# Kernel tuning notes

Measured on AMD Instinct MI355X. Metric: run time of the kernel, lower is better.

The kernel has to match this reference:

```python
import jax, jax.numpy as jnp
import numpy as np

DIM = 1024
N_SRC = 4096
N_TGT = 4096


def setup_inputs() -> dict:
    key = jax.random.key(0)
    ks = jax.random.split(key, 7)
    scale = 1.0 / np.sqrt(DIM)
    return {
        "source": jax.random.normal(ks[0], (N_SRC, DIM), dtype=jnp.float32),
        "target": jax.random.normal(ks[1], (N_TGT, DIM), dtype=jnp.float32),
        "W_src": jax.random.uniform(ks[2], (DIM, DIM), minval=-scale, maxval=scale, dtype=jnp.float32),
        "b_src": jax.random.uniform(ks[3], (DIM,), minval=-scale, maxval=scale, dtype=jnp.float32),
        "W_tgt": jax.random.uniform(ks[4], (DIM, DIM), minval=-scale, maxval=scale, dtype=jnp.float32),
        "b_tgt": jax.random.uniform(ks[5], (DIM,), minval=-scale, maxval=scale, dtype=jnp.float32),
        "temperature": jnp.array(1.0, dtype=jnp.float32),
    }


def reference(source, target, W_src, b_src, W_tgt, b_tgt, temperature):
    # Linear projections (torch Linear: x @ W.T + b)
    sp = source @ W_src.T + b_src            # [N, d]
    tp = target @ W_tgt.T + b_tgt            # [M, d]
    sq_s = jnp.sum(sp * sp, axis=-1, keepdims=True)   # [N, 1]
    sq_t = jnp.sum(tp * tp, axis=-1)                  # [M]
    d2 = sq_s + sq_t[None, :] - 2.0 * (sp @ tp.T)     # [N, M]
    cost = jnp.sqrt(jnp.maximum(d2, 0.0))
    # Softmin-style kernel, row-normalized over target entries
    K = jnp.exp(-cost / temperature)
    K = K / jnp.sum(K, axis=1, keepdims=True)
    aligned_source = K @ target                       # [N, d]
    return aligned_source, K
```

## Files before the change

kernel.cpp:

```cpp
#include <hip/hip_runtime.h>
#include <stdint.h>

#define DIM  1024
#define NSRC 4096
#define NTGT 4096

typedef __bf16 bf16_t;
typedef bf16_t bf16x8 __attribute__((ext_vector_type(8)));
typedef float  fx4    __attribute__((ext_vector_type(4)));

static __device__ __forceinline__ unsigned short f2bf(float f) {
  union { float f; uint32_t u; } v; v.f = f;
  return (unsigned short)((v.u + 0x7FFFu + ((v.u >> 16) & 1u)) >> 16);
}
static __device__ __forceinline__ float bf2f(unsigned short h) {
  union { uint32_t u; float f; } v; v.u = ((uint32_t)h) << 16;
  return v.f;
}

static __device__ __forceinline__ void gl_lds16(const unsigned short* g, unsigned short* l) {
  __builtin_amdgcn_global_load_lds(
      (__attribute__((address_space(1))) const void*)g,
      (__attribute__((address_space(3))) void*)l, 16, 0, 0);
}


__global__ void k_convert_all(const float* __restrict__ s, const float* __restrict__ t,
                              const float* __restrict__ w0, const float* __restrict__ w1,
                              unsigned short* __restrict__ sb, unsigned short* __restrict__ tb,
                              unsigned short* __restrict__ wb0, unsigned short* __restrict__ wb1) {
  int b = blockIdx.x;
  const float* in; unsigned short* out; int idx;
  if (b < 4096)      { in = s;  out = sb;  idx = b * 256 + threadIdx.x; }
  else if (b < 8192) { in = t;  out = tb;  idx = (b - 4096) * 256 + threadIdx.x; }
  else if (b < 9216) { in = w0; out = wb0; idx = (b - 8192) * 256 + threadIdx.x; }
  else               { in = w1; out = wb1; idx = (b - 9216) * 256 + threadIdx.x; }
  float4 v = ((const float4*)in)[idx];
  ushort4 o;
  o.x = f2bf(v.x); o.y = f2bf(v.y); o.z = f2bf(v.z); o.w = f2bf(v.w);
  ((ushort4*)out)[idx] = o;
}

__global__ void k_transpose_bf16(const float* __restrict__ in, unsigned short* __restrict__ out,
                                 int R, int C) {
  __shared__ unsigned short tile[32][33];
  int c0 = blockIdx.x * 32, r0 = blockIdx.y * 32;
  int tx = threadIdx.x, ty = threadIdx.y;
  for (int i = ty; i < 32; i += 8) {
    int row = r0 + i;
    int p = row & 63;
    int tr = (row & ~63) | ((p >> 2) | ((p & 3) << 4));
    tile[i][tx] = f2bf(in[(size_t)tr * C + c0 + tx]);
  }
  __syncthreads();
  for (int i = ty; i < 32; i += 8)
    out[(size_t)(c0 + i) * R + r0 + tx] = tile[tx][i];
}

__global__ void k_finalize(const float* __restrict__ P, float* __restrict__ aligned,
                           const unsigned short* __restrict__ Eb, float* __restrict__ Kf,
                           const float* __restrict__ rs) {
  const int b = blockIdx.x;
  const int lane = threadIdx.x & 63, w = threadIdx.x >> 6;
  const int src = ((lane & 15) << 2) | (lane >> 4);
  if (b < 4096) {
    const size_t stride = (size_t)NSRC * DIM;
#pragma unroll
    for (int it = 0; it < 4; ++it) {
      int idx = b * 16 + w * 4 + it;
      size_t base = (size_t)idx * 64;
      float r = 1.0f / rs[idx >> 4];
      float v = (P[base + lane] + P[base + stride + lane] +
                 P[base + 2 * stride + lane] + P[base + 3 * stride + lane]) * r;
      aligned[base + lane] = __shfl(v, src, 64);
    }
  } else {
    const int bb = b - 4096;
#pragma unroll
    for (int it = 0; it < 8; ++it) {
      int idx = bb * 32 + w * 8 + it;
      size_t base = (size_t)idx * 64;
      float r = 1.0f / rs[idx >> 6];
      float v = bf2f(Eb[base + lane]) * r;
      Kf[base + lane] = __shfl(v, src, 64);
    }
  }
}

template <int EPI>
__global__ void __launch_bounds__(256)
k_gemm(const unsigned short* __restrict__ A0, const unsigned short* __restrict__ B0,
       const unsigned short* __restrict__ A1, const unsigned short* __restrict__ B1,
       int N, int K,
       const float* __restrict__ bias0, const float* __restrict__ bias1,
       unsigned short* __restrict__ Cb0, unsigned short* __restrict__ Cb1,
       float* __restrict__ Cf,
       const float* __restrict__ sqs, const float* __restrict__ sqt,
       const float* __restrict__ tempPtr,
       float* __restrict__ red0, float* __restrict__ red1,
       int KS) {
  __shared__ unsigned short ldsA[128 * 32];
  __shared__ unsigned short ldsB[128 * 32];
  __shared__ float rsum[128];

  const unsigned short* A = A0;
  const unsigned short* B = B0;
  const float* bias = bias0;
  unsigned short* Cb = Cb0;
  float* red = red0;
  int k0 = 0, k1 = K;
  if constexpr (EPI == 0) {
    if (blockIdx.z) { A = A1; B = B1; bias = bias1; Cb = Cb1; red = red1; }
  }
  if constexpr (EPI == 3) { k0 = blockIdx.z * KS; k1 = k0 + KS; }

  const int m0 = blockIdx.y * 128;
  const int n0 = blockIdx.x * 128;
  const int tid  = threadIdx.x;
  const int lane = tid & 63;
  const int wv   = tid >> 6;
  const int wm   = wv >> 1, wn = wv & 1;

  const int c0    = wv * 2;
  const int srow  = lane >> 2;
  const int skoff = (lane & 3) * 8;
  const unsigned short* ag[2]; const unsigned short* bg[2];
  unsigned short* la[2]; unsigned short* lb[2];
#pragma unroll
  for (int j = 0; j < 2; ++j) {
    int c = c0 + j;
    ag[j] = A + (size_t)(m0 + c * 16 + srow) * K + skoff;
    bg[j] = B + (size_t)(n0 + c * 16 + srow) * K + skoff;
    la[j] = ldsA + c * 512;
    lb[j] = ldsB + c * 512;
  }

  const fx4 fzero = {0.f, 0.f, 0.f, 0.f};
  fx4 acc[4][4];
#pragma unroll
  for (int i = 0; i < 4; ++i)
#pragma unroll
    for (int j = 0; j < 4; ++j) acc[i][j] = fzero;

  const int frow = lane & 15;
  const int kq   = lane >> 4;
  const int aoff = (wm * 64 + frow) * 32 + kq * 8;
  const int boff = (wn * 64 + frow) * 32 + kq * 8;

  for (int ko = k0; ko < k1; ko += 32) {
    gl_lds16(ag[0] + ko, la[0]);
    gl_lds16(ag[1] + ko, la[1]);
    gl_lds16(bg[0] + ko, lb[0]);
    gl_lds16(bg[1] + ko, lb[1]);
    __syncthreads();
    bf16x8 af[4], bfr[4];
#pragma unroll
    for (int t = 0; t < 4; ++t) af[t]  = *(const bf16x8*)(ldsA + aoff + t * 512);
#pragma unroll
    for (int t = 0; t < 4; ++t) bfr[t] = *(const bf16x8*)(ldsB + boff + t * 512);
#pragma unroll
    for (int i = 0; i < 4; ++i)
#pragma unroll
      for (int j = 0; j < 4; ++j)
        acc[i][j] = __builtin_amdgcn_mfma_f32_16x16x32_bf16(af[i], bfr[j], acc[i][j], 0, 0, 0);
    __syncthreads();
  }

  const int gcol0 = n0 + wn * 64 + frow;
  const int scol  = n0 + wn * 64 + frow * 4;

  if constexpr (EPI == 0 || EPI == 1) {
    if (tid < 128) rsum[tid] = 0.f;
    __syncthreads();
    float invT = 0.f;
    if constexpr (EPI == 1) invT = 1.0f / tempPtr[0];
#pragma unroll
    for (int i = 0; i < 4; ++i)
#pragma unroll
      for (int r = 0; r < 4; ++r) {
        const int lrow = wm * 64 + kq * 4 + i * 16 + r;
        const int gm   = m0 + lrow;
        float si = 0.f;
        if constexpr (EPI == 1) si = sqs[gm];
        float racc = 0.f;
        ushort4 o;
        unsigned short* op = (unsigned short*)&o;
#pragma unroll
        for (int j = 0; j < 4; ++j) {
          float e;
          if constexpr (EPI == 0) {
            e = acc[i][j][r] + bias[gcol0 + j * 16];
          } else {
            float d2 = si + sqt[gcol0 + j * 16] - 2.0f * acc[i][j][r];
            float c = sqrtf(fmaxf(d2, 0.0f));
            e = __expf(-c * invT);
          }
          unsigned short eb = f2bf(e);
          op[j] = eb;
          float ev = bf2f(eb);
          racc += (EPI == 0) ? ev * ev : ev;
        }
        *(ushort4*)(Cb + (size_t)gm * N + scol) = o;
        racc += __shfl_xor(racc, 1, 64);
        racc += __shfl_xor(racc, 2, 64);
        racc += __shfl_xor(racc, 4, 64);
        racc += __shfl_xor(racc, 8, 64);
        if (frow == 0) atomicAdd(&rsum[lrow], racc);
      }
    __syncthreads();
    if (tid < 128) atomicAdd(&red[m0 + tid], rsum[tid]);
  } else {
    float* Pz = Cf + (size_t)blockIdx.z * NSRC * DIM;
#pragma unroll
    for (int i = 0; i < 4; ++i)
#pragma unroll
      for (int r = 0; r < 4; ++r) {
        const int gm = m0 + wm * 64 + kq * 4 + i * 16 + r;
        float4 v = make_float4(acc[i][0][r], acc[i][1][r], acc[i][2][r], acc[i][3][r]);
        *(float4*)(Pz + (size_t)gm * N + scol) = v;
      }
  }
}

extern "C" void kernel_launch(void* const* d_in, const int* in_sizes, int n_in,
                              void* d_out, int out_size, void* d_ws, size_t ws_size,
                              hipStream_t stream) {
  const float* source = (const float*)d_in[0];
  const float* target = (const float*)d_in[1];
  const float* W_src  = (const float*)d_in[2];
  const float* b_src  = (const float*)d_in[3];
  const float* W_tgt  = (const float*)d_in[4];
  const float* b_tgt  = (const float*)d_in[5];
  const float* temp   = (const float*)d_in[6];

  float* out     = (float*)d_out;
  float* aligned = out;
  float* Kout    = out + (size_t)NSRC * DIM;
  float* parts   = Kout;

  char* ws = (char*)d_ws;
  unsigned short* src_b  = (unsigned short*)(ws + 0);
  unsigned short* tgt_b  = (unsigned short*)(ws + 8388608);
  unsigned short* Wsrc_b = (unsigned short*)(ws + 16777216);
  unsigned short* Wtgt_b = (unsigned short*)(ws + 18874368);
  unsigned short* sp_b   = (unsigned short*)(ws + 20971520);
  unsigned short* tp_b   = (unsigned short*)(ws + 29360128);
  unsigned short* tgtT_b = (unsigned short*)(ws + 37748736);
  unsigned short* E_b    = (unsigned short*)(ws + 46137344);
  float* sq_s  = (float*)(ws + 79691776);
  float* sq_t  = (float*)(ws + 79708160);
  float* rsums = (float*)(ws + 79724544);

  hipMemsetAsync(sq_s, 0, 3 * NSRC * sizeof(float), stream);

  k_convert_all<<<10240, 256, 0, stream>>>(source, target, W_src, W_tgt,
                                           src_b, tgt_b, Wsrc_b, Wtgt_b);
  k_transpose_bf16<<<dim3(DIM / 32, NTGT / 32), dim3(32, 8), 0, stream>>>(target, tgtT_b, NTGT, DIM);

  k_gemm<0><<<dim3(DIM / 128, NSRC / 128, 2), 256, 0, stream>>>(
      src_b, Wsrc_b, tgt_b, Wtgt_b, DIM, DIM, b_src, b_tgt, sp_b, tp_b,
      nullptr, nullptr, nullptr, nullptr, sq_s, sq_t, 0);

  k_gemm<1><<<dim3(NTGT / 128, NSRC / 128, 1), 256, 0, stream>>>(
      sp_b, tp_b, nullptr, nullptr, NTGT, DIM, nullptr, nullptr, E_b, nullptr,
      nullptr, sq_s, sq_t, temp, rsums, nullptr, 0);

  k_gemm<3><<<dim3(DIM / 128, NSRC / 128, 4), 256, 0, stream>>>(
      E_b, tgtT_b, nullptr, nullptr, DIM, NTGT, nullptr, nullptr, nullptr, nullptr,
      parts, nullptr, nullptr, nullptr, nullptr, nullptr, NTGT / 4);

  k_finalize<<<12288, 256, 0, stream>>>(parts, aligned, E_b, Kout, rsums);
}
```

Measured before the change: 314.5 us.

## Add 256x256 pipelined score GEMM kernel and halve split-K for aligned GEMM

Replaces the generic 128x128 score GEMM (EPI==1) with a dedicated 512-thread, 256x256-tile kernel. It double-buffers LDS through direct global-to-LDS loads, interleaves staging with MFMA groups under explicit waitcnt and barrier control, and raises wave priority during MFMA. This aims at better data reuse and latency hiding for the largest GEMM. The K@target GEMM split-K drops from 4 to 2, which halves the partial-sum traffic, and the finalize step is split into two separate kernels. The tradeoffs are higher register and LDS pressure from the large tile, and fewer blocks for the split-K GEMM.

```diff
diff --git a/kernel.cpp b/kernel.cpp
--- a/kernel.cpp
+++ b/kernel.cpp
@@ -57,33 +57,34 @@
     out[(size_t)(c0 + i) * R + r0 + tx] = tile[tx][i];
 }
 
-__global__ void k_finalize(const float* __restrict__ P, float* __restrict__ aligned,
-                           const unsigned short* __restrict__ Eb, float* __restrict__ Kf,
-                           const float* __restrict__ rs) {
+__global__ void k_finalize_aligned(const float* __restrict__ P, float* __restrict__ aligned,
+                                   const float* __restrict__ rs) {
   const int b = blockIdx.x;
   const int lane = threadIdx.x & 63, w = threadIdx.x >> 6;
   const int src = ((lane & 15) << 2) | (lane >> 4);
-  if (b < 4096) {
-    const size_t stride = (size_t)NSRC * DIM;
-#pragma unroll
-    for (int it = 0; it < 4; ++it) {
-      int idx = b * 16 + w * 4 + it;
-      size_t base = (size_t)idx * 64;
-      float r = 1.0f / rs[idx >> 4];
-      float v = (P[base + lane] + P[base + stride + lane] +
-                 P[base + 2 * stride + lane] + P[base + 3 * stride + lane]) * r;
-      aligned[base + lane] = __shfl(v, src, 64);
-    }
-  } else {
-    const int bb = b - 4096;
-#pragma unroll
-    for (int it = 0; it < 8; ++it) {
-      int idx = bb * 32 + w * 8 + it;
-      size_t base = (size_t)idx * 64;
-      float r = 1.0f / rs[idx >> 6];
-      float v = bf2f(Eb[base + lane]) * r;
-      Kf[base + lane] = __shfl(v, src, 64);
-    }
+  const size_t stride = (size_t)NSRC * DIM;
+#pragma unroll
+  for (int it = 0; it < 4; ++it) {
+    int idx = b * 16 + w * 4 + it;
+    size_t base = (size_t)idx * 64;
+    float r = 1.0f / rs[idx >> 4];
+    float v = (P[base + lane] + P[base + stride + lane]) * r;
+    aligned[base + lane] = __shfl(v, src, 64);
+  }
+}
+
+__global__ void k_finalize_K(const unsigned short* __restrict__ Eb, float* __restrict__ Kf,
+                             const float* __restrict__ rs) {
+  const int b = blockIdx.x;
+  const int lane = threadIdx.x & 63, w = threadIdx.x >> 6;
+  const int src = ((lane & 15) << 2) | (lane >> 4);
+#pragma unroll
+  for (int it = 0; it < 8; ++it) {
+    int idx = b * 32 + w * 8 + it;
+    size_t base = (size_t)idx * 64;
+    float r = 1.0f / rs[idx >> 6];
+    float v = bf2f(Eb[base + lane]) * r;
+    Kf[base + lane] = __shfl(v, src, 64);
   }
 }
 
@@ -169,36 +170,25 @@
   const int gcol0 = n0 + wn * 64 + frow;
   const int scol  = n0 + wn * 64 + frow * 4;
 
-  if constexpr (EPI == 0 || EPI == 1) {
+  if constexpr (EPI == 0) {
     if (tid < 128) rsum[tid] = 0.f;
     __syncthreads();
-    float invT = 0.f;
-    if constexpr (EPI == 1) invT = 1.0f / tempPtr[0];
 #pragma unroll
     for (int i = 0; i < 4; ++i)
 #pragma unroll
       for (int r = 0; r < 4; ++r) {
         const int lrow = wm * 64 + kq * 4 + i * 16 + r;
         const int gm   = m0 + lrow;
-        float si = 0.f;
-        if constexpr (EPI == 1) si = sqs[gm];
         float racc = 0.f;
         ushort4 o;
         unsigned short* op = (unsigned short*)&o;
 #pragma unroll
         for (int j = 0; j < 4; ++j) {
-          float e;
-          if constexpr (EPI == 0) {
-            e = acc[i][j][r] + bias[gcol0 + j * 16];
-          } else {
-            float d2 = si + sqt[gcol0 + j * 16] - 2.0f * acc[i][j][r];
-            float c = sqrtf(fmaxf(d2, 0.0f));
-            e = __expf(-c * invT);
-          }
+          float e = acc[i][j][r] + bias[gcol0 + j * 16];
           unsigned short eb = f2bf(e);
           op[j] = eb;
           float ev = bf2f(eb);
-          racc += (EPI == 0) ? ev * ev : ev;
+          racc += ev * ev;
         }
         *(ushort4*)(Cb + (size_t)gm * N + scol) = o;
         racc += __shfl_xor(racc, 1, 64);
@@ -222,6 +212,151 @@
   }
 }
 
+__global__ void __launch_bounds__(512, 2)
+k_score256(const unsigned short* __restrict__ A, const unsigned short* __restrict__ B,
+           unsigned short* __restrict__ Eb,
+           const float* __restrict__ sqs, const float* __restrict__ sqt,
+           const float* __restrict__ tempPtr, float* __restrict__ rsums) {
+  __shared__ unsigned short ldsA[32768];
+  __shared__ unsigned short ldsB[32768];
+
+  const int tid = threadIdx.x;
+  const int lane = tid & 63, w = tid >> 6;
+  const int wm = w >> 2, wn = w & 3;
+  const int fr = lane & 15, kq = lane >> 4;
+  const int m0 = blockIdx.y * 256, n0 = blockIdx.x * 256;
+
+  const int rin = lane >> 2;
+  const int cs  = ((lane & 3) * 8) ^ ((lane >> 5) ? 16 : 0);
+  const size_t aoff0 = (size_t)(m0 + w * 16 + rin) * DIM + cs;
+  const size_t aoff1 = (size_t)(m0 + (8 + w) * 16 + rin) * DIM + cs;
+  const size_t boff0 = (size_t)(n0 + w * 16 + rin) * DIM + cs;
+  const size_t boff1 = (size_t)(n0 + (8 + w) * 16 + rin) * DIM + cs;
+
+  const int roA = fr * 32 + ((kq * 8) ^ ((fr & 8) ? 16 : 0));
+
+#define STAGE_A(buf, ksb, kk) do { \
+    gl_lds16(A + aoff0 + (kk) + (ksb) * 32, ldsA + (buf) * 16384 + (ksb) * 8192 + w * 512); \
+    gl_lds16(A + aoff1 + (kk) + (ksb) * 32, ldsA + (buf) * 16384 + (ksb) * 8192 + (8 + w) * 512); \
+  } while (0)
+#define STAGE_B(buf, ksb, kk) do { \
+    gl_lds16(B + boff0 + (kk) + (ksb) * 32, ldsB + (buf) * 16384 + (ksb) * 8192 + w * 512); \
+    gl_lds16(B + boff1 + (kk) + (ksb) * 32, ldsB + (buf) * 16384 + (ksb) * 8192 + (8 + w) * 512); \
+  } while (0)
+
+  const fx4 fz = {0.f, 0.f, 0.f, 0.f};
+  fx4 acc[8][4];
+#pragma unroll
+  for (int i = 0; i < 8; ++i)
+#pragma unroll
+    for (int j = 0; j < 4; ++j) acc[i][j] = fz;
+
+  bf16x8 a[8], b0v, b1v;
+
+#define LDA8(buf, ks) do { _Pragma("unroll") \
+    for (int i = 0; i < 8; ++i) \
+      a[i] = *(const bf16x8*)(ldsA + (buf) * 16384 + (ks) * 8192 + (wm * 8 + i) * 512 + roA); \
+  } while (0)
+#define LDB2(buf, ks, jh) do { \
+    b0v = *(const bf16x8*)(ldsB + (buf) * 16384 + (ks) * 8192 + (wn * 4 + (jh) * 2) * 512 + roA); \
+    b1v = *(const bf16x8*)(ldsB + (buf) * 16384 + (ks) * 8192 + (wn * 4 + (jh) * 2 + 1) * 512 + roA); \
+  } while (0)
+#define MFMA16(jh) do { _Pragma("unroll") \
+    for (int i = 0; i < 8; ++i) { \
+      acc[i][(jh) * 2]     = __builtin_amdgcn_mfma_f32_16x16x32_bf16(a[i], b0v, acc[i][(jh) * 2], 0, 0, 0); \
+      acc[i][(jh) * 2 + 1] = __builtin_amdgcn_mfma_f32_16x16x32_bf16(a[i], b1v, acc[i][(jh) * 2 + 1], 0, 0, 0); \
+    } } while (0)
+#define BAR()   __builtin_amdgcn_s_barrier()
+#define SB0()   __builtin_amdgcn_sched_barrier(0)
+#define LGKM0() asm volatile("s_waitcnt lgkmcnt(0)" ::: "memory")
+#define VM6()   asm volatile("s_waitcnt vmcnt(6)" ::: "memory")
+
+  STAGE_A(0, 0, 0);  STAGE_B(0, 0, 0);  STAGE_A(0, 1, 0);  STAGE_B(0, 1, 0);
+  STAGE_A(1, 0, 64); STAGE_B(1, 0, 64); STAGE_A(1, 1, 64);
+  VM6();
+  SB0(); BAR();
+
+#pragma unroll 1
+  for (int it = 0; it < 8; ++it) {
+    const int kk1 = it * 128 + 64;
+    const int kk2 = (it * 128 + 128) & (DIM - 1);
+    const int kk3 = (it * 128 + 192) & (DIM - 1);
+    LDA8(0, 0); LDB2(0, 0, 0); STAGE_B(1, 1, kk1);
+    SB0(); BAR(); LGKM0();
+    __builtin_amdgcn_s_setprio(1); MFMA16(0); __builtin_amdgcn_s_setprio(0);
+    SB0(); BAR();
+    LDB2(0, 0, 1); STAGE_A(0, 0, kk2);
+    SB0(); BAR(); LGKM0();
+    __builtin_amdgcn_s_setprio(1); MFMA16(1); __builtin_amdgcn_s_setprio(0);
+    SB0(); BAR();
+    LDA8(0, 1); LDB2(0, 1, 0); STAGE_B(0, 0, kk2);
+    SB0(); BAR(); LGKM0();
+    __builtin_amdgcn_s_setprio(1); MFMA16(0); __builtin_amdgcn_s_setprio(0);
+    SB0(); BAR();
+    LDB2(0, 1, 1); STAGE_A(0, 1, kk2);
+    SB0(); BAR(); LGKM0();
+    __builtin_amdgcn_s_setprio(1); MFMA16(1); __builtin_amdgcn_s_setprio(0);
+    VM6();
+    SB0(); BAR();
+    LDA8(1, 0); LDB2(1, 0, 0); STAGE_B(0, 1, kk2);
+    SB0(); BAR(); LGKM0();
+    __builtin_amdgcn_s_setprio(1); MFMA16(0); __builtin_amdgcn_s_setprio(0);
+    SB0(); BAR();
+    LDB2(1, 0, 1); STAGE_A(1, 0, kk3);
+    SB0(); BAR(); LGKM0();
+    __builtin_amdgcn_s_setprio(1); MFMA16(1); __builtin_amdgcn_s_setprio(0);
+    SB0(); BAR();
+    LDA8(1, 1); LDB2(1, 1, 0); STAGE_B(1, 0, kk3);
+    SB0(); BAR(); LGKM0();
+    __builtin_amdgcn_s_setprio(1); MFMA16(0); __builtin_amdgcn_s_setprio(0);
+    SB0(); BAR();
+    LDB2(1, 1, 1); STAGE_A(1, 1, kk3);
+    SB0(); BAR(); LGKM0();
+    __builtin_amdgcn_s_setprio(1); MFMA16(1); __builtin_amdgcn_s_setprio(0);
+    VM6();
+    SB0(); BAR();
+  }
+  asm volatile("s_waitcnt vmcnt(0)" ::: "memory");
+  __syncthreads();
+
+  const float invT = 1.0f / tempPtr[0];
+  const int gcol0 = n0 + wn * 64 + fr;
+  const int scol  = n0 + wn * 64 + fr * 4;
+#pragma unroll
+  for (int i = 0; i < 8; ++i)
+#pragma unroll
+    for (int r = 0; r < 4; ++r) {
+      const int lrow = wm * 128 + i * 16 + kq * 4 + r;
+      const int gm = m0 + lrow;
+      const float si = sqs[gm];
+      float racc = 0.f;
+      ushort4 o; unsigned short* op = (unsigned short*)&o;
+#pragma unroll
+      for (int j = 0; j < 4; ++j) {
+        float d2 = si + sqt[gcol0 + j * 16] - 2.0f * acc[i][j][r];
+        float c = sqrtf(fmaxf(d2, 0.0f));
+        unsigned short eb = f2bf(__expf(-c * invT));
+        op[j] = eb;
+        racc += bf2f(eb);
+      }
+      *(ushort4*)(Eb + (size_t)gm * NTGT + scol) = o;
+      racc += __shfl_xor(racc, 1, 64);
+      racc += __shfl_xor(racc, 2, 64);
+      racc += __shfl_xor(racc, 4, 64);
+      racc += __shfl_xor(racc, 8, 64);
+      if (fr == 0) atomicAdd(&rsums[gm], racc);
+    }
+#undef STAGE_A
+#undef STAGE_B
+#undef LDA8
+#undef LDB2
+#undef MFMA16
+#undef BAR
+#undef SB0
+#undef LGKM0
+#undef VM6
+}
+
 extern "C" void kernel_launch(void* const* d_in, const int* in_sizes, int n_in,
                               void* d_out, int out_size, void* d_ws, size_t ws_size,
                               hipStream_t stream) {
@@ -261,13 +396,13 @@
       src_b, Wsrc_b, tgt_b, Wtgt_b, DIM, DIM, b_src, b_tgt, sp_b, tp_b,
       nullptr, nullptr, nullptr, nullptr, sq_s, sq_t, 0);
 
-  k_gemm<1><<<dim3(NTGT / 128, NSRC / 128, 1), 256, 0, stream>>>(
-      sp_b, tp_b, nullptr, nullptr, NTGT, DIM, nullptr, nullptr, E_b, nullptr,
-      nullptr, sq_s, sq_t, temp, rsums, nullptr, 0);
-
-  k_gemm<3><<<dim3(DIM / 128, NSRC / 128, 4), 256, 0, stream>>>(
+  k_score256<<<dim3(NTGT / 256, NSRC / 256), 512, 0, stream>>>(
+      sp_b, tp_b, E_b, sq_s, sq_t, temp, rsums);
+
+  k_gemm<3><<<dim3(DIM / 128, NSRC / 128, 2), 256, 0, stream>>>(
       E_b, tgtT_b, nullptr, nullptr, DIM, NTGT, nullptr, nullptr, nullptr, nullptr,
-      parts, nullptr, nullptr, nullptr, nullptr, nullptr, NTGT / 4);
-
-  k_finalize<<<12288, 256, 0, stream>>>(parts, aligned, E_b, Kout, rsums);
-}
+      parts, nullptr, nullptr, nullptr, nullptr, nullptr, NTGT / 2);
+
+  k_finalize_aligned<<<4096, 256, 0, stream>>>(parts, aligned, rsums);
+  k_finalize_K<<<8192, 256, 0, stream>>>(E_b, Kout, rsums);
+}
```

Result: faster. 296.9 us (-5.6%).
